# Kernel optimization log

Hardware: AMD Instinct MI355X
Metric: run time of the kernel (lower is better)

## Reference

```python
import jax, jax.numpy as jnp
import numpy as np


def setup_inputs() -> dict:
    key = jax.random.key(0)
    ks = jax.random.split(key, 6)
    B, S, D, E, F, C = 4, 2048, 1024, 8, 4096, 512
    return {
        "x": jax.random.normal(ks[0], (B, S, D), dtype=jnp.float32),
        "router": jax.random.normal(ks[1], (D, E), dtype=jnp.float32) * (1.0 / np.sqrt(D)),
        "w1": jax.random.normal(ks[2], (E, D, F), dtype=jnp.float32) * (1.0 / np.sqrt(D)),
        "b1": jnp.zeros((E, F), dtype=jnp.float32),
        "w2": jax.random.normal(ks[3], (E, F, D), dtype=jnp.float32) * (1.0 / np.sqrt(F)),
        "b2": jnp.zeros((E, D), dtype=jnp.float32),
        "capacity": C,
    }


def reference(x, router, w1, b1, w2, b2, capacity):
    # x: (B,S,D); router: (D,E); per-expert FFN weights stacked on E.
    B, S, D = x.shape
    # Gate: softmax over experts, then each expert picks its top-C tokens.
    logits = jnp.einsum('bsd,de->bse', x, router)            # (B,S,E)
    affinity = jax.nn.softmax(logits, axis=-1)               # (B,S,E)
    gating, index = jax.lax.top_k(jnp.transpose(affinity, (0, 2, 1)), capacity)  # (B,E,C)
    # Dispatch: gather token features per (expert, slot). Equivalent to the
    # one-hot einsum 'becs,bsd->becd' in the original (same math, true gather).
    x_in = jax.vmap(lambda xb, ib: xb[ib])(x, index)         # (B,E,C,D)
    # Per-expert GPT2 FFN: Linear -> GELU -> Linear (grouped GEMMs over E).
    h = jax.nn.gelu(jnp.einsum('becd,edf->becf', x_in, w1) + b1[None, :, None, :],
                    approximate=False)                        # (B,E,C,F)
    x_e = jnp.einsum('becf,efd->becd', h, w2) + b2[None, :, None, :]  # (B,E,C,D)
    # Combine: weighted scatter-add back to token positions. Equivalent to
    # einsum 'becs,bec,becd->bsd' with the one-hot dispatch mask.
    weighted = gating[..., None] * x_e                       # (B,E,C,D)
    out = jax.vmap(
        lambda ib, vb: jnp.zeros((S, D), x.dtype).at[ib.reshape(-1)].add(vb.reshape(-1, D))
    )(index, weighted)                                       # (B,S,D)
    return out
```

## Files before the change

kernel.cpp:

```cpp
#include <hip/hip_runtime.h>
#include <hip/hip_bf16.h>

#define B_ 4
#define S_ 2048
#define D_ 1024
#define E_ 8
#define F_ 4096
#define C_ 512
#define BE_ (B_*E_)

typedef __attribute__((ext_vector_type(8))) short bf16x8;
typedef __attribute__((ext_vector_type(4))) float f32x4;
typedef unsigned short u16;

#define MFMA16 __builtin_amdgcn_mfma_f32_16x16x32_bf16

static constexpr size_t OFF_AFF  = 0;
static constexpr size_t OFF_IDX  = 262144;
static constexpr size_t OFF_GATE = 327680;
static constexpr size_t OFF_XIN  = 393216;
static constexpr size_t OFF_WT1  = OFF_XIN + (size_t)BE_*C_*D_*2;
static constexpr size_t OFF_WT2  = OFF_WT1 + (size_t)E_*F_*D_*2;
static constexpr size_t OFF_H    = OFF_WT2 + (size_t)E_*D_*F_*2;
static constexpr size_t WS_NEED  = OFF_H   + (size_t)BE_*C_*F_*2;

static __device__ __forceinline__ u16 f2bf(float x) {
  __hip_bfloat16 h = __float2bfloat16(x);
  return *reinterpret_cast<u16*>(&h);
}

static __device__ __forceinline__ void gload16(const void* g, void* l) {
  __builtin_amdgcn_global_load_lds(
      (const __attribute__((address_space(1))) unsigned int*)g,
      (__attribute__((address_space(3))) unsigned int*)l, 16, 0, 0);
}

__global__ void router_kernel(const float* __restrict__ x,
                              const float* __restrict__ router,
                              float* __restrict__ aff) {
  int t = blockIdx.x;
  int b = t / S_, s = t % S_;
  int lane = threadIdx.x;
  const float* xrow = x + (size_t)t * D_;
  float acc[E_];
#pragma unroll
  for (int e = 0; e < E_; ++e) acc[e] = 0.f;
  for (int i = 0; i < D_/64; ++i) {
    int d = lane + i*64;
    float xv = xrow[d];
    const float* r = router + (size_t)d * E_;
#pragma unroll
    for (int e = 0; e < E_; ++e) acc[e] += xv * r[e];
  }
#pragma unroll
  for (int e = 0; e < E_; ++e) {
    float v = acc[e];
    for (int off = 32; off; off >>= 1) v += __shfl_down(v, off);
    acc[e] = v;
  }
  if (lane == 0) {
    float mx = acc[0];
#pragma unroll
    for (int e = 1; e < E_; ++e) mx = fmaxf(mx, acc[e]);
    float ev[E_]; float sum = 0.f;
#pragma unroll
    for (int e = 0; e < E_; ++e) { ev[e] = expf(acc[e] - mx); sum += ev[e]; }
    float inv = 1.0f / sum;
#pragma unroll
    for (int e = 0; e < E_; ++e) aff[((size_t)(b*E_ + e))*S_ + s] = ev[e]*inv;
  }
}

__global__ void topk_kernel(const float* __restrict__ aff,
                            int* __restrict__ idxb, float* __restrict__ gateb) {
  __shared__ unsigned long long keys[S_];
  int be = blockIdx.x;
  const float* a = aff + (size_t)be * S_;
  int tid = threadIdx.x;
  for (int i = tid; i < S_; i += 1024) {
    unsigned vb = __float_as_uint(a[i]);
    keys[i] = ((unsigned long long)(~vb) << 32) | (unsigned)i;
  }
  __syncthreads();
  for (int k = 2; k <= S_; k <<= 1) {
    for (int j = k >> 1; j > 0; j >>= 1) {
      for (int i = tid; i < S_; i += 1024) {
        int ixj = i ^ j;
        if (ixj > i) {
          unsigned long long ka = keys[i], kb = keys[ixj];
          bool up = ((i & k) == 0);
          if ((ka > kb) == up) { keys[i] = kb; keys[ixj] = ka; }
        }
      }
      __syncthreads();
    }
  }
  for (int c = tid; c < C_; c += 1024) {
    unsigned long long kk = keys[c];
    idxb[be*C_ + c]  = (int)(kk & 0xffffffffu);
    gateb[be*C_ + c] = __uint_as_float(~(unsigned)(kk >> 32));
  }
}

__global__ void gather_kernel(const float* __restrict__ x,
                              const int* __restrict__ idxb,
                              u16* __restrict__ x_in) {
  int rid = blockIdx.x;
  int be = rid >> 9;
  int b = be >> 3;
  int tok = idxb[rid];
  const float4* src = (const float4*)(x + ((size_t)(b * S_ + tok)) * D_);
  ushort4* dst = (ushort4*)(x_in + (size_t)rid * D_);
  int t = threadIdx.x;
#pragma unroll
  for (int i = 0; i < 2; ++i) {
    float4 v = src[t + i*128];
    ushort4 o;
    o.x = f2bf(v.x); o.y = f2bf(v.y); o.z = f2bf(v.z); o.w = f2bf(v.w);
    dst[t + i*128] = o;
  }
}

__global__ void trans_kernel(const float* __restrict__ src,
                             u16* __restrict__ dst, int RI, int RJ) {
  __shared__ float t[64][65];
  int e  = blockIdx.z;
  int j0 = blockIdx.x * 64;
  int i0 = blockIdx.y * 64;
  const float* s = src + (size_t)e * RI * RJ;
  u16* d = dst + (size_t)e * RI * RJ;
  int tid = threadIdx.x;
#pragma unroll
  for (int it = 0; it < 4; ++it) {
    int fid = it*256 + tid;
    int r = fid >> 4, c4 = fid & 15;
    float4 v = *(const float4*)(s + (size_t)(i0 + r) * RJ + j0 + c4*4);
    t[r][c4*4+0] = v.x; t[r][c4*4+1] = v.y; t[r][c4*4+2] = v.z; t[r][c4*4+3] = v.w;
  }
  __syncthreads();
#pragma unroll
  for (int it = 0; it < 4; ++it) {
    int fid = it*256 + tid;
    int rn = fid >> 4, c4 = fid & 15;
    ushort4 o;
    o.x = f2bf(t[c4*4+0][rn]); o.y = f2bf(t[c4*4+1][rn]);
    o.z = f2bf(t[c4*4+2][rn]); o.w = f2bf(t[c4*4+3][rn]);
    *(ushort4*)(d + (size_t)(j0 + rn) * RI + i0 + c4*4) = o;
  }
}

template<int EPI, int N, int K, int NBLK>
__global__ __launch_bounds__(512, 2)
void gemm8_kernel(const u16* __restrict__ A, const u16* __restrict__ Bt,
                  const float* __restrict__ bias, void* __restrict__ outp,
                  const int* __restrict__ idxb, const float* __restrict__ gateb,
                  float* __restrict__ dout) {
  constexpr int NT = K / 64;
  __shared__ __align__(16) char lds[131072];
  const int tid  = threadIdx.x;
  const int wave = tid >> 6, lane = tid & 63;
  const int wm = wave >> 2, wn = wave & 3;
  const int l15 = lane & 15, chi = lane >> 4;

  const int bid = blockIdx.x;
  const int e   = bid & 7;
  const int r   = bid >> 3;
  const int nb  = r % NBLK;
  const int rm  = r / NBLK;
  const int mb  = rm & 1;
  const int b   = rm >> 1;
  const int be  = b * E_ + e;
  const int m0  = mb * 256;
  const int n0  = nb * 256;

  const u16* Ab  = A  + (size_t)be * C_ * K + (size_t)m0 * K;
  const u16* Bb  = Bt + (size_t)e  * N  * K + (size_t)n0 * K;
  const u16* Ab2 = Ab + (size_t)128 * K;
  const u16* Bb2 = Bb + (size_t)128 * K;

  const int sr = tid >> 3, scn = tid & 7;
  const size_t off0 = (size_t)sr * K + (size_t)((scn ^ (sr & 7)) << 3);
  const size_t off1 = off0 + (size_t)64 * K;
  const int ldsd = tid * 16;

#define STAGE(tt, so, gb) \
  if ((tt) < NT) { \
    const u16* g_ = (gb) + (size_t)(tt) * 64; \
    char* l_ = lds + (((tt) & 1) * 65536) + (so); \
    gload16(g_ + off0, l_ + ldsd); \
    gload16(g_ + off1, l_ + 8192 + ldsd); \
  }

  const int q7  = l15 & 7;
  const int ch0 = ((chi    ) ^ q7) << 4;
  const int ch1 = ((4 + chi) ^ q7) << 4;
  const int aoff = wm * 16384 + l15 * 128;
  const int boff = 32768 + (wn >> 1) * 16384 + (wn & 1) * 8192 + l15 * 128;

  f32x4 acc[8][4];
#pragma unroll
  for (int i = 0; i < 8; ++i)
#pragma unroll
    for (int j = 0; j < 4; ++j) acc[i][j] = (f32x4){0.f,0.f,0.f,0.f};

  STAGE(0, 0,     Ab);
  STAGE(0, 16384, Ab2);
  STAGE(0, 32768, Bb);
  STAGE(0, 49152, Bb2);
  STAGE(1, 32768, Bb);
  STAGE(1, 49152, Bb2);
  asm volatile("s_waitcnt vmcnt(4)" ::: "memory");
  __builtin_amdgcn_s_barrier();

  bf16x8 af[2][4], bA[2][2], bB[2][2];
  for (int t = 0; t < NT; ++t) {
    const char* cb = lds + (t & 1) * 65536;
#pragma unroll
    for (int m = 0; m < 4; ++m) {
      af[0][m] = *(const bf16x8*)(cb + aoff + m*2048 + ch0);
      af[1][m] = *(const bf16x8*)(cb + aoff + m*2048 + ch1);
    }
#pragma unroll
    for (int n = 0; n < 2; ++n) {
      bA[0][n] = *(const bf16x8*)(cb + boff + n*2048 + ch0);
      bA[1][n] = *(const bf16x8*)(cb + boff + n*2048 + ch1);
    }
    STAGE(t+1, 0, Ab);
    asm volatile("s_waitcnt lgkmcnt(8)" ::: "memory");
    __builtin_amdgcn_s_barrier();
    asm volatile("s_waitcnt lgkmcnt(0)" ::: "memory");
    __builtin_amdgcn_s_setprio(1);
#pragma unroll
    for (int m = 0; m < 4; ++m)
#pragma unroll
      for (int n = 0; n < 2; ++n) {
        acc[m][n] = MFMA16(af[0][m], bA[0][n], acc[m][n], 0, 0, 0);
        acc[m][n] = MFMA16(af[1][m], bA[1][n], acc[m][n], 0, 0, 0);
      }
    __builtin_amdgcn_s_setprio(0);
    __builtin_amdgcn_s_barrier();
#pragma unroll
    for (int n = 0; n < 2; ++n) {
      bB[0][n] = *(const bf16x8*)(cb + boff + (2+n)*2048 + ch0);
      bB[1][n] = *(const bf16x8*)(cb + boff + (2+n)*2048 + ch1);
    }
    STAGE(t+1, 16384, Ab2);
    __builtin_amdgcn_s_barrier();
    asm volatile("s_waitcnt lgkmcnt(0)" ::: "memory");
    __builtin_amdgcn_s_setprio(1);
#pragma unroll
    for (int m = 0; m < 4; ++m)
#pragma unroll
      for (int n = 0; n < 2; ++n) {
        acc[m][2+n] = MFMA16(af[0][m], bB[0][n], acc[m][2+n], 0, 0, 0);
        acc[m][2+n] = MFMA16(af[1][m], bB[1][n], acc[m][2+n], 0, 0, 0);
      }
    __builtin_amdgcn_s_setprio(0);
    __builtin_amdgcn_s_barrier();
#pragma unroll
    for (int m = 0; m < 4; ++m) {
      af[0][m] = *(const bf16x8*)(cb + aoff + (4+m)*2048 + ch0);
      af[1][m] = *(const bf16x8*)(cb + aoff + (4+m)*2048 + ch1);
    }
    STAGE(t+2, 32768, Bb);
    __builtin_amdgcn_s_barrier();
    asm volatile("s_waitcnt lgkmcnt(0)" ::: "memory");
    __builtin_amdgcn_s_setprio(1);
#pragma unroll
    for (int m = 0; m < 4; ++m)
#pragma unroll
      for (int n = 0; n < 2; ++n) {
        acc[4+m][2+n] = MFMA16(af[0][m], bB[0][n], acc[4+m][2+n], 0, 0, 0);
        acc[4+m][2+n] = MFMA16(af[1][m], bB[1][n], acc[4+m][2+n], 0, 0, 0);
      }
    __builtin_amdgcn_s_setprio(0);
    __builtin_amdgcn_s_barrier();
    STAGE(t+2, 49152, Bb2);
    if (t < NT-2) {
      asm volatile("s_waitcnt vmcnt(4)" ::: "memory");
    } else if (t == NT-2) {
      asm volatile("s_waitcnt vmcnt(0)" ::: "memory");
    }
    __builtin_amdgcn_s_barrier();
    __builtin_amdgcn_s_setprio(1);
#pragma unroll
    for (int m = 0; m < 4; ++m)
#pragma unroll
      for (int n = 0; n < 2; ++n) {
        acc[4+m][n] = MFMA16(af[0][m], bA[0][n], acc[4+m][n], 0, 0, 0);
        acc[4+m][n] = MFMA16(af[1][m], bA[1][n], acc[4+m][n], 0, 0, 0);
      }
    __builtin_amdgcn_s_setprio(0);
    __builtin_amdgcn_s_barrier();
  }
#undef STAGE

  const int r4 = lane >> 4;
  if (EPI == 0) {
    __hip_bfloat16* hb = (__hip_bfloat16*)outp + (size_t)be * C_ * N;
    const float* bias_e = bias + e * N;
#pragma unroll
    for (int mi = 0; mi < 8; ++mi) {
#pragma unroll
      for (int j = 0; j < 4; ++j) {
        int row = m0 + wm*128 + mi*16 + r4*4 + j;
        __hip_bfloat16* hrow = hb + (size_t)row * N;
#pragma unroll
        for (int ni = 0; ni < 4; ++ni) {
          int col = n0 + wn*64 + ni*16 + l15;
          float v = acc[mi][ni][j] + bias_e[col];
          float g = 0.5f * v * (1.0f + erff(v * 0.70710678118654752f));
          hrow[col] = __float2bfloat16(g);
        }
      }
    }
  } else {
    const float* bias_e = bias + e * N;
    int bb = be >> 3;
#pragma unroll
    for (int mi = 0; mi < 8; ++mi) {
#pragma unroll
      for (int j = 0; j < 4; ++j) {
        int rowl = m0 + wm*128 + mi*16 + r4*4 + j;
        int tok = idxb[be*C_ + rowl];
        float gt = gateb[be*C_ + rowl];
        float* orow = dout + ((size_t)bb * S_ + tok) * (size_t)D_;
#pragma unroll
        for (int ni = 0; ni < 4; ++ni) {
          int col = n0 + wn*64 + ni*16 + l15;
          float v = (acc[mi][ni][j] + bias_e[col]) * gt;
          atomicAdd(orow + col, v);
        }
      }
    }
  }
}

extern "C" void kernel_launch(void* const* d_in, const int* in_sizes, int n_in,
                              void* d_out, int out_size, void* d_ws, size_t ws_size,
                              hipStream_t stream) {
  const float* x      = (const float*)d_in[0];
  const float* router = (const float*)d_in[1];
  const float* w1     = (const float*)d_in[2];
  const float* b1     = (const float*)d_in[3];
  const float* w2     = (const float*)d_in[4];
  const float* b2     = (const float*)d_in[5];
  float* out = (float*)d_out;

  if (ws_size < WS_NEED) return;

  char* ws = (char*)d_ws;
  float* aff   = (float*)(ws + OFF_AFF);
  int*   idxb  = (int*)(ws + OFF_IDX);
  float* gateb = (float*)(ws + OFF_GATE);
  u16*   x_in  = (u16*)(ws + OFF_XIN);
  u16*   wt1   = (u16*)(ws + OFF_WT1);
  u16*   wt2   = (u16*)(ws + OFF_WT2);
  u16*   h     = (u16*)(ws + OFF_H);

  router_kernel<<<B_*S_, 64, 0, stream>>>(x, router, aff);
  topk_kernel<<<BE_, 1024, 0, stream>>>(aff, idxb, gateb);
  gather_kernel<<<BE_*C_, 128, 0, stream>>>(x, idxb, x_in);
  trans_kernel<<<dim3(F_/64, D_/64, E_), 256, 0, stream>>>(w1, wt1, D_, F_);
  trans_kernel<<<dim3(D_/64, F_/64, E_), 256, 0, stream>>>(w2, wt2, F_, D_);
  hipMemsetAsync(d_out, 0, (size_t)out_size * sizeof(float), stream);

  gemm8_kernel<0, F_, D_, F_/256><<<E_*(F_/256)*2*B_, 512, 0, stream>>>(
      x_in, wt1, b1, (void*)h, nullptr, nullptr, nullptr);
  gemm8_kernel<1, D_, F_, D_/256><<<E_*(D_/256)*2*B_, 512, 0, stream>>>(
      h, wt2, b2, nullptr, idxb, gateb, out);
}
```

Before: 492.3 us.

## Use smaller-tile unpipelined GEMM1 kernel with tanh-approx GELU epilogue

Replaces the first expert GEMM's 256x256, 512-thread pipelined kernel with a simpler 128x128-tile, 256-thread kernel that allows more blocks per CU. It also swaps the exact erf GELU for a tanh-style approximation computed through a sigmoid with a fast exp. The second GEMM keeps the old kernel with its scatter-add epilogue. The new kernel has no software pipelining: each K step loads and then barriers, so memory latency may be exposed, and the GELU approximation introduces small numerical differences.

Result: faster. 466.6 us (-5.2%).

```diff
diff --git a/kernel.cpp b/kernel.cpp
--- a/kernel.cpp
+++ b/kernel.cpp
@@ -27,6 +27,11 @@
 static __device__ __forceinline__ u16 f2bf(float x) {
   __hip_bfloat16 h = __float2bfloat16(x);
   return *reinterpret_cast<u16*>(&h);
+}
+
+static __device__ __forceinline__ float gelu_fast(float v) {
+  float y = 1.5957691216f * (v + 0.044715f * v * v * v);
+  return v / (1.0f + __expf(-y));
 }
 
 static __device__ __forceinline__ void gload16(const void* g, void* l) {
@@ -149,10 +154,96 @@
   }
 }
 
-template<int EPI, int N, int K, int NBLK>
+template<int N, int K, int NBLK>
+__global__ __launch_bounds__(256, 4)
+void gemm1_kernel(const u16* __restrict__ A, const u16* __restrict__ Bt,
+                  const float* __restrict__ bias, __hip_bfloat16* __restrict__ outp) {
+  __shared__ __align__(16) char lds[32768];
+  char* ldsA = lds;
+  char* ldsB = lds + 16384;
+  const int tid  = threadIdx.x;
+  const int wave = tid >> 6, lane = tid & 63;
+
+  const int bid = blockIdx.x;
+  const int e   = bid & 7;
+  const int r   = bid >> 3;
+  const int nb  = r % NBLK;
+  const int rm  = r / NBLK;
+  const int mb  = rm & 3;
+  const int b   = rm >> 2;
+  const int be  = b * E_ + e;
+  const int m0  = mb * 128;
+  const int n0  = nb * 128;
+
+  const u16* Ab = A  + (size_t)be * C_ * K + (size_t)m0 * K;
+  const u16* Bb = Bt + (size_t)e  * N  * K + (size_t)n0 * K;
+
+  f32x4 acc[4][4];
+#pragma unroll
+  for (int i = 0; i < 4; ++i)
+#pragma unroll
+    for (int j = 0; j < 4; ++j) acc[i][j] = (f32x4){0.f,0.f,0.f,0.f};
+
+  const int wr = wave >> 1, wc = wave & 1;
+  const int chi = lane >> 4;
+  const int l15 = lane & 15;
+
+  for (int kt = 0; kt < K/64; ++kt) {
+    const int k0 = kt * 64;
+#pragma unroll
+    for (int i = 0; i < 4; ++i) {
+      int slot = i*256 + tid;
+      int row = slot >> 3, c = slot & 7;
+      int sc = (c ^ (row & 7)) << 3;
+      gload16(Ab + (size_t)row * K + k0 + sc, ldsA + (i*256 + wave*64)*16);
+      gload16(Bb + (size_t)row * K + k0 + sc, ldsB + (i*256 + wave*64)*16);
+    }
+    __syncthreads();
+    bf16x8 af[2][4], bfr[2][4];
+#pragma unroll
+    for (int kk = 0; kk < 2; ++kk) {
+#pragma unroll
+      for (int mi = 0; mi < 4; ++mi) {
+        int row = wr*64 + mi*16 + l15;
+        int ch  = kk*4 + chi;
+        af[kk][mi] = *(const bf16x8*)(ldsA + row*128 + (((ch ^ (row & 7)) << 4)));
+        int rowb = wc*64 + mi*16 + l15;
+        bfr[kk][mi] = *(const bf16x8*)(ldsB + rowb*128 + (((ch ^ (rowb & 7)) << 4)));
+      }
+    }
+#pragma unroll
+    for (int kk = 0; kk < 2; ++kk)
+#pragma unroll
+      for (int mi = 0; mi < 4; ++mi)
+#pragma unroll
+        for (int ni = 0; ni < 4; ++ni)
+          acc[mi][ni] = MFMA16(af[kk][mi], bfr[kk][ni], acc[mi][ni], 0, 0, 0);
+    __syncthreads();
+  }
+
+  const int r4 = lane >> 4;
+  __hip_bfloat16* hb = outp + (size_t)be * C_ * N;
+  const float* bias_e = bias + e * N;
+#pragma unroll
+  for (int mi = 0; mi < 4; ++mi) {
+#pragma unroll
+    for (int j = 0; j < 4; ++j) {
+      int row = m0 + wr*64 + mi*16 + r4*4 + j;
+      __hip_bfloat16* hrow = hb + (size_t)row * N;
+#pragma unroll
+      for (int ni = 0; ni < 4; ++ni) {
+        int col = n0 + wc*64 + ni*16 + l15;
+        float v = acc[mi][ni][j] + bias_e[col];
+        hrow[col] = __float2bfloat16(gelu_fast(v));
+      }
+    }
+  }
+}
+
+template<int N, int K, int NBLK>
 __global__ __launch_bounds__(512, 2)
-void gemm8_kernel(const u16* __restrict__ A, const u16* __restrict__ Bt,
-                  const float* __restrict__ bias, void* __restrict__ outp,
+void gemm2_kernel(const u16* __restrict__ A, const u16* __restrict__ Bt,
+                  const float* __restrict__ bias,
                   const int* __restrict__ idxb, const float* __restrict__ gateb,
                   float* __restrict__ dout) {
   constexpr int NT = K / 64;
@@ -296,41 +387,21 @@
 #undef STAGE
 
   const int r4 = lane >> 4;
-  if (EPI == 0) {
-    __hip_bfloat16* hb = (__hip_bfloat16*)outp + (size_t)be * C_ * N;
-    const float* bias_e = bias + e * N;
-#pragma unroll
-    for (int mi = 0; mi < 8; ++mi) {
-#pragma unroll
-      for (int j = 0; j < 4; ++j) {
-        int row = m0 + wm*128 + mi*16 + r4*4 + j;
-        __hip_bfloat16* hrow = hb + (size_t)row * N;
-#pragma unroll
-        for (int ni = 0; ni < 4; ++ni) {
-          int col = n0 + wn*64 + ni*16 + l15;
-          float v = acc[mi][ni][j] + bias_e[col];
-          float g = 0.5f * v * (1.0f + erff(v * 0.70710678118654752f));
-          hrow[col] = __float2bfloat16(g);
-        }
-      }
-    }
-  } else {
-    const float* bias_e = bias + e * N;
-    int bb = be >> 3;
-#pragma unroll
-    for (int mi = 0; mi < 8; ++mi) {
-#pragma unroll
-      for (int j = 0; j < 4; ++j) {
-        int rowl = m0 + wm*128 + mi*16 + r4*4 + j;
-        int tok = idxb[be*C_ + rowl];
-        float gt = gateb[be*C_ + rowl];
-        float* orow = dout + ((size_t)bb * S_ + tok) * (size_t)D_;
-#pragma unroll
-        for (int ni = 0; ni < 4; ++ni) {
-          int col = n0 + wn*64 + ni*16 + l15;
-          float v = (acc[mi][ni][j] + bias_e[col]) * gt;
-          atomicAdd(orow + col, v);
-        }
+  const float* bias_e = bias + e * N;
+  int bb = be >> 3;
+#pragma unroll
+  for (int mi = 0; mi < 8; ++mi) {
+#pragma unroll
+    for (int j = 0; j < 4; ++j) {
+      int rowl = m0 + wm*128 + mi*16 + r4*4 + j;
+      int tok = idxb[be*C_ + rowl];
+      float gt = gateb[be*C_ + rowl];
+      float* orow = dout + ((size_t)bb * S_ + tok) * (size_t)D_;
+#pragma unroll
+      for (int ni = 0; ni < 4; ++ni) {
+        int col = n0 + wn*64 + ni*16 + l15;
+        float v = (acc[mi][ni][j] + bias_e[col]) * gt;
+        atomicAdd(orow + col, v);
       }
     }
   }
@@ -365,8 +436,8 @@
   trans_kernel<<<dim3(D_/64, F_/64, E_), 256, 0, stream>>>(w2, wt2, F_, D_);
   hipMemsetAsync(d_out, 0, (size_t)out_size * sizeof(float), stream);
 
-  gemm8_kernel<0, F_, D_, F_/256><<<E_*(F_/256)*2*B_, 512, 0, stream>>>(
-      x_in, wt1, b1, (void*)h, nullptr, nullptr, nullptr);
-  gemm8_kernel<1, D_, F_, D_/256><<<E_*(D_/256)*2*B_, 512, 0, stream>>>(
-      h, wt2, b2, nullptr, idxb, gateb, out);
-}
+  gemm1_kernel<F_, D_, F_/128><<<E_*(F_/128)*4*B_, 256, 0, stream>>>(
+      x_in, wt1, b1, (__hip_bfloat16*)h);
+  gemm2_kernel<D_, F_, D_/256><<<E_*(D_/256)*2*B_, 512, 0, stream>>>(
+      h, wt2, b2, idxb, gateb, out);
+}
```
